# Optimization experiments

Measured on AMD Instinct MI355X. Metric: run time of the kernel, lower is better.

The kernel has to match this reference:

```python
import jax, jax.numpy as jnp
import numpy as np
import math

D_MODEL = 1024
N_HEADS = 16
B, S = 4, 2048

def _xavier(key, shape):
    fan_out, fan_in = shape
    limit = math.sqrt(6.0 / (fan_in + fan_out))
    return jax.random.uniform(key, shape, jnp.float32, -limit, limit)

def setup_inputs() -> dict:
    key = jax.random.key(0)
    kx, kqkv, ko = jax.random.split(key, 3)
    x = jax.random.normal(kx, (B, S, D_MODEL), dtype=jnp.float32)
    W_qkv = _xavier(kqkv, (3 * D_MODEL, D_MODEL))
    W_o = _xavier(ko, (D_MODEL, D_MODEL))
    return {"x": x, "W_qkv": W_qkv, "W_o": W_o}

def reference(x, W_qkv, W_o):
    Bx, Sx, D = x.shape
    H = N_HEADS
    d_h = D // H
    T = jnp.einsum('bsd,ed->bse', x, W_qkv)          # (B,S,3D)
    Q, K, V = jnp.split(T, 3, axis=-1)
    # (B,S,D) -> (B,H,S,d_h)
    Q = Q.reshape(Bx, Sx, H, d_h).transpose(0, 2, 1, 3)
    K = K.reshape(Bx, Sx, H, d_h).transpose(0, 2, 1, 3)
    V = V.reshape(Bx, Sx, H, d_h).transpose(0, 2, 1, 3)
    scores = jnp.einsum('bhqd,bhkd->bhqk', Q, K) / jnp.sqrt(jnp.float32(d_h))
    attn = jax.nn.softmax(scores, axis=-1)
    out = jnp.einsum('bhqk,bhkd->bhqd', attn, V)
    out = out.transpose(0, 2, 1, 3).reshape(Bx, Sx, D)
    Y = jnp.einsum('bsd,ed->bse', out, W_o)
    return Y
```

## Files before the change

### kernel.cpp

```cpp
#include <hip/hip_runtime.h>
#include <stdint.h>

#define SS 2048

typedef __attribute__((ext_vector_type(8))) short short8;
typedef __attribute__((ext_vector_type(4))) float f32x4;
typedef __attribute__((ext_vector_type(16))) float f32x16;

static __device__ __forceinline__ unsigned short f2bf(float f) {
    uint32_t u = __builtin_bit_cast(uint32_t, f);
    u += 0x7fffu + ((u >> 16) & 1u);
    return (unsigned short)(u >> 16);
}

static __device__ __forceinline__ uint32_t cvtpk(float lo, float hi) {
    uint32_t r;
    asm("v_cvt_pk_bf16_f32 %0, %1, %2" : "=v"(r) : "v"(lo), "v"(hi));
    return r;
}

static __device__ __forceinline__ void async16(const unsigned short* g, unsigned short* l) {
    __builtin_amdgcn_global_load_lds(
        (const __attribute__((address_space(1))) uint32_t*)g,
        (__attribute__((address_space(3))) uint32_t*)l, 16, 0, 0);
}

__global__ void cast_f32_bf16(const float* __restrict__ src, unsigned short* __restrict__ dst, int n) {
    int i = (blockIdx.x * 256 + threadIdx.x) * 4;
    if (i >= n) return;
    float4 v = *(const float4*)(src + i);
    ushort4 o;
    o.x = f2bf(v.x); o.y = f2bf(v.y); o.z = f2bf(v.z); o.w = f2bf(v.w);
    *(ushort4*)(dst + i) = o;
}

template<int MODE>
__global__ void gemm_bt(const unsigned short* __restrict__ A,
                        const unsigned short* __restrict__ Bm,
                        void* __restrict__ Cout,
                        unsigned short* __restrict__ Vt,
                        int K) {
    __shared__ unsigned short As[128 * 64];
    __shared__ unsigned short Bs[128 * 64];
    const int t = threadIdx.x;
    const int w = t >> 6, l = t & 63;
    const int wm = w >> 1, wn = w & 1;
    const int l15 = l & 15, l4 = l >> 4;
    const int m0 = blockIdx.x * 128, n0 = blockIdx.y * 128;
    const int srow = t >> 3;
    const int scol = (t & 7) * 8;

    f32x4 acc[4][4] = {};

    for (int k0 = 0; k0 < K; k0 += 64) {
#pragma unroll
        for (int r = 0; r < 4; ++r) {
            int row = r * 32 + srow;
            async16(A + (size_t)(m0 + row) * K + k0 + scol, (unsigned short*)&As[row * 64 + scol]);
        }
#pragma unroll
        for (int r = 0; r < 4; ++r) {
            int row = r * 32 + srow;
            async16(Bm + (size_t)(n0 + row) * K + k0 + scol, (unsigned short*)&Bs[row * 64 + scol]);
        }
        __syncthreads();
#pragma unroll
        for (int kk = 0; kk < 64; kk += 32) {
            short8 af[4], bfr[4];
#pragma unroll
            for (int m = 0; m < 4; ++m)
                af[m] = *(const short8*)&As[(wm * 64 + m * 16 + l15) * 64 + kk + l4 * 8];
#pragma unroll
            for (int n = 0; n < 4; ++n)
                bfr[n] = *(const short8*)&Bs[(wn * 64 + n * 16 + l15) * 64 + kk + l4 * 8];
#pragma unroll
            for (int m = 0; m < 4; ++m)
#pragma unroll
                for (int n = 0; n < 4; ++n)
                    acc[m][n] = __builtin_amdgcn_mfma_f32_16x16x32_bf16(af[m], bfr[n], acc[m][n], 0, 0, 0);
        }
        __syncthreads();
    }

#pragma unroll
    for (int m = 0; m < 4; ++m) {
        int rbase = m0 + wm * 64 + m * 16 + l4 * 4;
#pragma unroll
        for (int n = 0; n < 4; ++n) {
            int c = n0 + wn * 64 + n * 16 + l15;
            f32x4 v = acc[m][n];
            if (MODE == 0) {
                if (c < 2048) {
                    float sc = (c < 1024) ? 0.18033688f : 1.0f;
                    unsigned short* T = (unsigned short*)Cout;
#pragma unroll
                    for (int r = 0; r < 4; ++r)
                        T[(size_t)(rbase + r) * 2048 + c] = f2bf(v[0 + r] * sc);
                } else {
                    int vv = c - 2048;
                    int hh = vv >> 6, d = vv & 63;
                    int bb = rbase >> 11, s = rbase & 2047;
                    ushort4 pk;
                    pk.x = f2bf(v[0]); pk.y = f2bf(v[1]); pk.z = f2bf(v[2]); pk.w = f2bf(v[3]);
                    *(ushort4*)&Vt[((size_t)(bb * 16 + hh) * 64 + d) * 2048 + s] = pk;
                }
            } else {
                float* C = (float*)Cout;
#pragma unroll
                for (int r = 0; r < 4; ++r)
                    C[(size_t)(rbase + r) * 1024 + c] = v[r];
            }
        }
    }
}

__global__ __launch_bounds__(256, 4) void attn_kernel(
        const unsigned short* __restrict__ Tqk,
        const unsigned short* __restrict__ Vt,
        unsigned short* __restrict__ Out) {
    __shared__ unsigned short Ks[2][64 * 64];
    __shared__ unsigned short Vs[2][64 * 64];
    const int t = threadIdx.x;
    const int w = t >> 6, l = t & 63;
    const int lq = l & 31, hfl = l >> 5;

    const int lin = blockIdx.x;
    const int j = lin >> 3;
    const int bh = (lin & 7) * 8 + (j & 7);
    const int qt = j >> 3;
    const int b = bh >> 4, hh = bh & 15;
    const int qrow = qt * 128 + w * 32 + lq;

    short8 qf[4];
    const size_t trow = ((size_t)b * SS + qrow) * 2048;
#pragma unroll
    for (int dc = 0; dc < 4; ++dc)
        qf[dc] = *(const short8*)&Tqk[trow + hh * 64 + dc * 16 + hfl * 8];

    char* KsB = (char*)Ks;
    char* VsB = (char*)Vs;

    const int srow = t >> 3;
    const int scb = (t & 7) << 4;
    const int ssw = scb ^ ((srow & 7) << 4);
    const int sel = scb >> 1;

    const unsigned short* kp0 = Tqk + (size_t)b * SS * 2048 + 1024 + hh * 64 + (size_t)srow * 2048 + sel;
    const unsigned short* kp1 = kp0 + 32 * 2048;
    const unsigned short* vp0 = Vt + (size_t)bh * 64 * 2048 + (size_t)srow * 2048 + sel;
    const unsigned short* vp1 = vp0 + 32 * 2048;

    int4 kr0, kr1, vr0, vr1;
#define ISSUE()                                                                      \
    kr0 = *(const int4*)kp0; kr1 = *(const int4*)kp1;                                \
    vr0 = *(const int4*)vp0; vr1 = *(const int4*)vp1;
#define WRITE(buf)                                                                   \
    {                                                                                \
        char* kb = KsB + (buf) * 8192;                                               \
        char* vb = VsB + (buf) * 8192;                                               \
        *(int4*)(kb + srow * 128 + ssw) = kr0;                                       \
        *(int4*)(kb + (srow + 32) * 128 + ssw) = kr1;                                \
        *(int4*)(vb + srow * 128 + ssw) = vr0;                                       \
        *(int4*)(vb + (srow + 32) * 128 + ssw) = vr1;                                \
    }

    f32x16 oacc[2] = {};
    float la0 = 0.f, la1 = 0.f, la2 = 0.f, la3 = 0.f;

    ISSUE();
    WRITE(0);
    __syncthreads();

    for (int it = 0; it < 32; ++it) {
        const int cur = it & 1;
        const char* kb = KsB + cur * 8192;
        const char* vb = VsB + cur * 8192;
        const bool more = (it < 31);
        if (more) {
            kp0 += 64 * 2048; kp1 += 64 * 2048;
            vp0 += 64;        vp1 += 64;
            ISSUE();
        }

        f32x16 sa[2] = {};
        __builtin_amdgcn_s_setprio(1);
#pragma unroll
        for (int kvt = 0; kvt < 2; ++kvt) {
            int row = kvt * 32 + lq;
#pragma unroll
            for (int dc = 0; dc < 4; ++dc) {
                short8 kf = *(const short8*)(kb + row * 128 + ((dc * 32 + hfl * 16) ^ ((row & 7) << 4)));
                sa[kvt] = __builtin_amdgcn_mfma_f32_32x32x16_bf16(kf, qf[dc], sa[kvt], 0, 0, 0);
            }
        }
        __builtin_amdgcn_s_setprio(0);

#pragma unroll
        for (int kvt = 0; kvt < 2; ++kvt)
#pragma unroll
            for (int r = 0; r < 16; r += 4) {
                float p0 = __builtin_amdgcn_exp2f(sa[kvt][r + 0]);
                float p1 = __builtin_amdgcn_exp2f(sa[kvt][r + 1]);
                float p2 = __builtin_amdgcn_exp2f(sa[kvt][r + 2]);
                float p3 = __builtin_amdgcn_exp2f(sa[kvt][r + 3]);
                sa[kvt][r + 0] = p0; la0 += p0;
                sa[kvt][r + 1] = p1; la1 += p1;
                sa[kvt][r + 2] = p2; la2 += p2;
                sa[kvt][r + 3] = p3; la3 += p3;
            }

        short8 pb[4];
#pragma unroll
        for (int c = 0; c < 4; ++c) {
            int f = c >> 1, r0 = (c & 1) * 8;
            uint32_t v0 = cvtpk(sa[f][r0 + 0], sa[f][r0 + 1]);
            uint32_t v1 = cvtpk(sa[f][r0 + 2], sa[f][r0 + 3]);
            uint32_t v2 = cvtpk(sa[f][r0 + 4], sa[f][r0 + 5]);
            uint32_t v3 = cvtpk(sa[f][r0 + 6], sa[f][r0 + 7]);
            asm("v_permlane32_swap_b32 %0, %1" : "+v"(v0), "+v"(v2));
            asm("v_permlane32_swap_b32 %0, %1" : "+v"(v1), "+v"(v3));
            union { uint32_t u[4]; short8 s; } pbu;
            pbu.u[0] = v0;
            pbu.u[1] = v1;
            pbu.u[2] = v2;
            pbu.u[3] = v3;
            pb[c] = pbu.s;
        }

        __builtin_amdgcn_s_setprio(1);
#pragma unroll
        for (int dt = 0; dt < 2; ++dt) {
            int row0 = dt * 32 + lq;
#pragma unroll
            for (int c = 0; c < 4; ++c) {
                short8 vf = *(const short8*)(vb + row0 * 128 + ((c * 32 + hfl * 16) ^ ((row0 & 7) << 4)));
                oacc[dt] = __builtin_amdgcn_mfma_f32_32x32x16_bf16(vf, pb[c], oacc[dt], 0, 0, 0);
            }
        }
        __builtin_amdgcn_s_setprio(0);

        if (more) { WRITE(cur ^ 1); }
        __syncthreads();
    }
#undef ISSUE
#undef WRITE

    float l_run = (la0 + la1) + (la2 + la3);
    l_run += __shfl_xor(l_run, 32);
    float inv = 1.0f / l_run;
    const size_t obase = ((size_t)b * SS + qrow) * 1024 + hh * 64;
#pragma unroll
    for (int dt = 0; dt < 2; ++dt)
#pragma unroll
        for (int r = 0; r < 16; ++r) {
            int d = dt * 32 + (r & 3) + 8 * (r >> 2) + 4 * hfl;
            Out[obase + d] = f2bf(oacc[dt][r] * inv);
        }
}

extern "C" void kernel_launch(void* const* d_in, const int* in_sizes, int n_in,
                              void* d_out, int out_size, void* d_ws, size_t ws_size,
                              hipStream_t stream) {
    const float* x    = (const float*)d_in[0];
    const float* wqkv = (const float*)d_in[1];
    const float* wo   = (const float*)d_in[2];

    unsigned short* ws  = (unsigned short*)d_ws;
    unsigned short* xb  = ws;
    unsigned short* w1  = ws + 8388608;
    unsigned short* w2  = ws + 11534336;
    unsigned short* vt  = ws + 12582912;
    unsigned short* ao  = ws + 20971520;
    unsigned short* tqk = (unsigned short*)d_out;

    cast_f32_bf16<<<8192, 256, 0, stream>>>(x, xb, 8388608);
    cast_f32_bf16<<<3072, 256, 0, stream>>>(wqkv, w1, 3145728);
    cast_f32_bf16<<<1024, 256, 0, stream>>>(wo, w2, 1048576);

    gemm_bt<0><<<dim3(64, 24), 256, 0, stream>>>(xb, w1, (void*)tqk, vt, 1024);
    attn_kernel<<<1024, 256, 0, stream>>>(tqk, vt, ao);
    gemm_bt<1><<<dim3(64, 8), 256, 0, stream>>>(ao, w2, d_out, nullptr, 1024);
}
```

Before: 190.4 us.

## Use async global-to-LDS K/V loads, MFMA row sums, and a single fused cast kernel

Three changes. The attention kernel now stages K/V tiles with global_load_lds async copies instead of loading into registers and writing to LDS afterwards, which cuts register pressure and the extra LDS write instructions. The softmax denominator is now accumulated by an MFMA of P against a vector of ones rather than by scalar adds plus a cross-lane shuffle, moving that work onto the matrix cores. The three f32-to-bf16 cast launches are merged into one kernel to save launch overhead, and the added full vmcnt(0) wait each iteration could limit overlap.

```diff
diff --git a/kernel.cpp b/kernel.cpp
--- a/kernel.cpp
+++ b/kernel.cpp
@@ -25,13 +25,20 @@
         (__attribute__((address_space(3))) uint32_t*)l, 16, 0, 0);
 }
 
-__global__ void cast_f32_bf16(const float* __restrict__ src, unsigned short* __restrict__ dst, int n) {
+__global__ void cast3(const float* __restrict__ a, const float* __restrict__ b,
+                      const float* __restrict__ c,
+                      unsigned short* __restrict__ da, unsigned short* __restrict__ db,
+                      unsigned short* __restrict__ dc_) {
     int i = (blockIdx.x * 256 + threadIdx.x) * 4;
-    if (i >= n) return;
-    float4 v = *(const float4*)(src + i);
+    const float* s;
+    unsigned short* d;
+    if (i < 8388608)        { s = a + i;              d = da + i; }
+    else if (i < 11534336)  { s = b + (i - 8388608);  d = db + (i - 8388608); }
+    else                    { s = c + (i - 11534336); d = dc_ + (i - 11534336); }
+    float4 v = *(const float4*)s;
     ushort4 o;
     o.x = f2bf(v.x); o.y = f2bf(v.y); o.z = f2bf(v.z); o.w = f2bf(v.w);
-    *(ushort4*)(dst + i) = o;
+    *(ushort4*)d = o;
 }
 
 template<int MODE>
@@ -140,46 +147,43 @@
     char* KsB = (char*)Ks;
     char* VsB = (char*)Vs;
 
-    const int srow = t >> 3;
-    const int scb = (t & 7) << 4;
-    const int ssw = scb ^ ((srow & 7) << 4);
-    const int sel = scb >> 1;
-
-    const unsigned short* kp0 = Tqk + (size_t)b * SS * 2048 + 1024 + hh * 64 + (size_t)srow * 2048 + sel;
-    const unsigned short* kp1 = kp0 + 32 * 2048;
-    const unsigned short* vp0 = Vt + (size_t)bh * 64 * 2048 + (size_t)srow * 2048 + sel;
-    const unsigned short* vp1 = vp0 + 32 * 2048;
-
-    int4 kr0, kr1, vr0, vr1;
-#define ISSUE()                                                                      \
-    kr0 = *(const int4*)kp0; kr1 = *(const int4*)kp1;                                \
-    vr0 = *(const int4*)vp0; vr1 = *(const int4*)vp1;
-#define WRITE(buf)                                                                   \
+    const int swcol = ((l & 7) ^ (l >> 3)) * 8;
+    const unsigned short* kga = Tqk + (size_t)b * SS * 2048 + 1024 + hh * 64
+                              + (size_t)(w * 16 + (l >> 3)) * 2048 + swcol;
+    const unsigned short* kgb = kga + 8 * 2048;
+    const unsigned short* vga = Vt + (size_t)bh * 64 * 2048
+                              + (size_t)(w * 16 + (l >> 3)) * 2048 + swcol;
+    const unsigned short* vgb = vga + 8 * 2048;
+    const int ldw = w * 16 * 128;
+
+#define STAGE(buf)                                                                   \
     {                                                                                \
-        char* kb = KsB + (buf) * 8192;                                               \
-        char* vb = VsB + (buf) * 8192;                                               \
-        *(int4*)(kb + srow * 128 + ssw) = kr0;                                       \
-        *(int4*)(kb + (srow + 32) * 128 + ssw) = kr1;                                \
-        *(int4*)(vb + srow * 128 + ssw) = vr0;                                       \
-        *(int4*)(vb + (srow + 32) * 128 + ssw) = vr1;                                \
+        char* kd = KsB + (buf) * 8192 + ldw;                                         \
+        char* vd = VsB + (buf) * 8192 + ldw;                                         \
+        async16(kga, (unsigned short*)kd);                                           \
+        async16(kgb, (unsigned short*)(kd + 1024));                                  \
+        async16(vga, (unsigned short*)vd);                                           \
+        async16(vgb, (unsigned short*)(vd + 1024));                                  \
     }
 
     f32x16 oacc[2] = {};
-    float la0 = 0.f, la1 = 0.f, la2 = 0.f, la3 = 0.f;
-
-    ISSUE();
-    WRITE(0);
+    f32x16 lacc = {};
+    short8 ones;
+#pragma unroll
+    for (int i = 0; i < 8; ++i) ones[i] = (short)0x3F80;
+
+    STAGE(0);
+    asm volatile("s_waitcnt vmcnt(0)" ::: "memory");
     __syncthreads();
 
     for (int it = 0; it < 32; ++it) {
         const int cur = it & 1;
         const char* kb = KsB + cur * 8192;
         const char* vb = VsB + cur * 8192;
-        const bool more = (it < 31);
-        if (more) {
-            kp0 += 64 * 2048; kp1 += 64 * 2048;
-            vp0 += 64;        vp1 += 64;
-            ISSUE();
+        if (it < 31) {
+            kga += 64 * 2048; kgb += 64 * 2048;
+            vga += 64;        vgb += 64;
+            STAGE(cur ^ 1);
         }
 
         f32x16 sa[2] = {};
@@ -198,16 +202,8 @@
 #pragma unroll
         for (int kvt = 0; kvt < 2; ++kvt)
 #pragma unroll
-            for (int r = 0; r < 16; r += 4) {
-                float p0 = __builtin_amdgcn_exp2f(sa[kvt][r + 0]);
-                float p1 = __builtin_amdgcn_exp2f(sa[kvt][r + 1]);
-                float p2 = __builtin_amdgcn_exp2f(sa[kvt][r + 2]);
-                float p3 = __builtin_amdgcn_exp2f(sa[kvt][r + 3]);
-                sa[kvt][r + 0] = p0; la0 += p0;
-                sa[kvt][r + 1] = p1; la1 += p1;
-                sa[kvt][r + 2] = p2; la2 += p2;
-                sa[kvt][r + 3] = p3; la3 += p3;
-            }
+            for (int r = 0; r < 16; ++r)
+                sa[kvt][r] = __builtin_amdgcn_exp2f(sa[kvt][r]);
 
         short8 pb[4];
 #pragma unroll
@@ -237,17 +233,17 @@
                 oacc[dt] = __builtin_amdgcn_mfma_f32_32x32x16_bf16(vf, pb[c], oacc[dt], 0, 0, 0);
             }
         }
+#pragma unroll
+        for (int c = 0; c < 4; ++c)
+            lacc = __builtin_amdgcn_mfma_f32_32x32x16_bf16(ones, pb[c], lacc, 0, 0, 0);
         __builtin_amdgcn_s_setprio(0);
 
-        if (more) { WRITE(cur ^ 1); }
+        asm volatile("s_waitcnt vmcnt(0)" ::: "memory");
         __syncthreads();
     }
-#undef ISSUE
-#undef WRITE
-
-    float l_run = (la0 + la1) + (la2 + la3);
-    l_run += __shfl_xor(l_run, 32);
-    float inv = 1.0f / l_run;
+#undef STAGE
+
+    float inv = 1.0f / lacc[0];
     const size_t obase = ((size_t)b * SS + qrow) * 1024 + hh * 64;
 #pragma unroll
     for (int dt = 0; dt < 2; ++dt)
@@ -273,10 +269,7 @@
     unsigned short* ao  = ws + 20971520;
     unsigned short* tqk = (unsigned short*)d_out;
 
-    cast_f32_bf16<<<8192, 256, 0, stream>>>(x, xb, 8388608);
-    cast_f32_bf16<<<3072, 256, 0, stream>>>(wqkv, w1, 3145728);
-    cast_f32_bf16<<<1024, 256, 0, stream>>>(wo, w2, 1048576);
-
+    cast3<<<12288, 256, 0, stream>>>(x, wqkv, wo, xb, w1, w2);
     gemm_bt<0><<<dim3(64, 24), 256, 0, stream>>>(xb, w1, (void*)tqk, vt, 1024);
     attn_kernel<<<1024, 256, 0, stream>>>(tqk, vt, ao);
     gemm_bt<1><<<dim3(64, 8), 256, 0, stream>>>(ao, w2, d_out, nullptr, 1024);
```

Measured after the change: 192.0 us. Within noise of the previous version (+0.8%).
